# Kernel tuning notes

Hardware: AMD Instinct MI355X
Metric: run time of the kernel (lower is better)

Reference implementation:

```python
import jax, jax.numpy as jnp
import numpy as np

BLANK = 0          # tf.nn.ctc_loss default blank_index (StringLookup reserves 0 for OOV)
PAD = 127          # padding_value = char_to_num.vocabulary_size()
NEG = -1e30        # log-space 'zero' (avoid -inf to keep grads NaN-free)
B, T, C, L = 1024, 256, 128, 32


def setup_inputs() -> dict:
    key = jax.random.key(0)
    k1, k2 = jax.random.split(key)
    # labels in [1, PAD-1]; none equal PAD so label_length == L (full-length labels)
    y_true = jax.random.randint(k1, (B, L), 1, PAD).astype(jnp.int32)
    y_pred = jax.random.normal(k2, (B, T, C), dtype=jnp.float32)
    return {"y_true": y_true, "y_pred": y_pred}


def _ctc_loss(y_true, y_pred):
    """Faithful jax version of tf.nn.ctc_loss(labels, logits, label_len, T,
    logits_time_major=False, blank_index=0): standard log-space alpha DP."""
    Bn, Tn, Cn = y_pred.shape
    Ln = y_true.shape[1]
    S = 2 * Ln + 1  # extended label length (blanks interleaved)

    logp = jax.nn.log_softmax(y_pred, axis=-1)                    # [B,T,C]

    # extended label sequence: blank, l1, blank, l2, ..., blank   # [B,S]
    ext = jnp.full((Bn, S), BLANK, dtype=y_true.dtype)
    ext = ext.at[:, 1::2].set(y_true)

    # log-probs gathered at extended-label symbols                # [B,T,S]
    lp_ext = jnp.take_along_axis(
        logp, jnp.broadcast_to(ext[:, None, :], (Bn, Tn, S)), axis=2)

    # label_length = count of non-padding entries (mirrors count_nonzero)
    label_len = jnp.sum(y_true != PAD, axis=1)                    # [B]

    # skip transition s-2 -> s allowed iff ext[s] is a non-blank differing
    # from ext[s-2]
    skip_ok = jnp.concatenate(
        [jnp.zeros((Bn, 2), bool),
         (ext[:, 2:] != BLANK) & (ext[:, 2:] != ext[:, :-2])], axis=1)  # [B,S]

    neg1 = jnp.full((Bn, 1), NEG, logp.dtype)
    neg2 = jnp.full((Bn, 2), NEG, logp.dtype)

    alpha0 = jnp.full((Bn, S), NEG, logp.dtype)
    alpha0 = alpha0.at[:, 0].set(lp_ext[:, 0, 0]).at[:, 1].set(lp_ext[:, 0, 1])

    def step(alpha, lp_t):  # alpha,[B,S]  lp_t,[B,S]
        a1 = jnp.concatenate([neg1, alpha[:, :-1]], axis=1)
        a2 = jnp.concatenate([neg2, alpha[:, :-2]], axis=1)
        a2 = jnp.where(skip_ok, a2, NEG)
        new = lp_t + jnp.logaddexp(jnp.logaddexp(alpha, a1), a2)
        return new, None

    lp_seq = jnp.transpose(lp_ext, (1, 0, 2))                     # [T,B,S]
    alphaT, _ = jax.lax.scan(step, alpha0, lp_seq[1:])            # [B,S]

    # total log-likelihood ends at last blank (2*len) or last label (2*len-1)
    bi = jnp.arange(Bn)
    e1 = 2 * label_len
    e2 = 2 * label_len - 1
    loglik = jnp.logaddexp(alphaT[bi, e1], alphaT[bi, e2])        # [B]
    return -loglik


def reference(y_true, y_pred):
    # The original layer returns y_pred and registers the loss via add_loss;
    # the compute-dominant quantity is the per-example CTC loss, returned here.
    return _ctc_loss(y_true, y_pred)
```

## Files before the change

kernel.cpp:

```cpp
#include <hip/hip_runtime.h>
#include <cstdint>


#define CTC_BLANK 0
#define CTC_PAD   127
#define NEG       (-1e30f)
#define LOG2E     1.44269504088896340736f
#define LN2       0.69314718055994530942f

constexpr int Bn = 1024, Tn = 256, Cn = 128, Ln = 32;
constexpr int NSLOT = Ln + 1;
constexpr int GSLOT = 34;
constexpr int GT_B  = GSLOT * Tn;

constexpr size_t WS_GT   = 0;
constexpr size_t WS_SLOT = (size_t)Bn * GT_B * 2;
constexpr size_t WS_S    = WS_SLOT + (size_t)Bn * Ln * 4;
constexpr size_t WS_NEED = WS_S + (size_t)Bn * 4;

__device__ __forceinline__ float fexp2(float x) { return __builtin_amdgcn_exp2f(x); }
__device__ __forceinline__ float flog2(float x) { return __builtin_amdgcn_logf(x); }

template <int CTRL>
__device__ __forceinline__ float dpp_add(float s) {
    int v = __builtin_amdgcn_update_dpp(0, __float_as_int(s), CTRL, 0xF, 0xF, true);
    return s + __int_as_float(v);
}
__device__ __forceinline__ float dpp_wave_shr1(float src, float old) {
    return __int_as_float(__builtin_amdgcn_update_dpp(
        __float_as_int(old), __float_as_int(src), 0x138, 0xF, 0xF, false));
}
__device__ __forceinline__ void gl_lds16(const float* g, float* l) {
    __builtin_amdgcn_global_load_lds(
        (const __attribute__((address_space(1))) uint32_t*)g,
        (__attribute__((address_space(3))) uint32_t*)l, 16, 0, 0);
}

__global__ __launch_bounds__(512, 8) void ctc_softmax_kernel(
        const int*   __restrict__ y_true,
        const float* __restrict__ y_pred,
        _Float16*    __restrict__ Gt,
        int*         __restrict__ slotO_arr,
        float*       __restrict__ Sglob)
{
    __shared__ int labels[Ln];
    __shared__ __align__(16) int cmap[Cn];
    __shared__ int used[Cn];
    __shared__ int wcnt[8];
    __shared__ float partS[16];

    const int b    = blockIdx.x;
    const int tid  = threadIdx.x;
    const int lane = tid & 63;
    const int wave = tid >> 6;
    const int half = lane >> 5;
    const int l32  = lane & 31;

    const float4* gsrc = (const float4*)(y_pred + (size_t)b * Tn * Cn);
    float4 xr0 = gsrc[tid];
    float4 xr1 = gsrc[512  + tid];
    float4 xr2 = gsrc[1024 + tid];
    float4 xr3 = gsrc[1536 + tid];

    if (tid < Ln) labels[tid] = y_true[b * Ln + tid];
    if (tid < Cn) used[tid] = 0;
    __syncthreads();
    if (tid == 0) used[CTC_BLANK] = 1;
    if (tid < Ln) used[labels[tid]] = 1;
    __syncthreads();
    {
        bool f = (tid < Cn) && (used[tid] != 0);
        unsigned long long m = __ballot(f);
        if (lane == 0) wcnt[wave] = __popcll(m);
        __syncthreads();
        int base = 0;
        for (int w = 0; w < wave; ++w) base += wcnt[w];
        if (tid < Cn)
            cmap[tid] = f ? (base + __popcll(m & ((1ull << lane) - 1ull))) : -1;
        __syncthreads();
    }

    const int4 cm = ((const int4*)cmap)[l32];
    _Float16* gt = Gt + (size_t)b * GT_B;
    const int rbase = tid >> 5;
    float acc = 0.f;

    #pragma unroll
    for (int j = 0; j < 16; ++j) {
        float4 x;
        if      ((j & 3) == 0) x = xr0;
        else if ((j & 3) == 1) x = xr1;
        else if ((j & 3) == 2) x = xr2;
        else                   x = xr3;
        if (j + 4 < 16) {
            float4 nx = gsrc[(j + 4) * 512 + tid];
            if      ((j & 3) == 0) xr0 = nx;
            else if ((j & 3) == 1) xr1 = nx;
            else if ((j & 3) == 2) xr2 = nx;
            else                   xr3 = nx;
        }
        const float e0 = x.x * LOG2E, e1 = x.y * LOG2E,
                    e2 = x.z * LOG2E, e3 = x.w * LOG2E;
        const int tcol = j * 16 + rbase;
        if (cm.x >= 0) gt[cm.x * Tn + tcol] = (_Float16)e0;
        if (cm.y >= 0) gt[cm.y * Tn + tcol] = (_Float16)e1;
        if (cm.z >= 0) gt[cm.z * Tn + tcol] = (_Float16)e2;
        if (cm.w >= 0) gt[cm.w * Tn + tcol] = (_Float16)e3;
        float s = fexp2(e0) + fexp2(e1) + fexp2(e2) + fexp2(e3);
        s = dpp_add<0x111>(s);
        s = dpp_add<0x112>(s);
        s = dpp_add<0x114>(s);
        s = dpp_add<0x118>(s);
        s = dpp_add<0x142>(s);
        acc += flog2(s);
    }
    if (l32 == 31) partS[wave * 2 + half] = acc;
    if (tid < Ln) slotO_arr[b * Ln + tid] = cmap[labels[tid]];
    __syncthreads();
    if (tid == 0) {
        float S = 0.f;
        #pragma unroll
        for (int j = 0; j < 16; ++j) S += partS[j];
        Sglob[b] = S;
    }
}

typedef __attribute__((ext_vector_type(4))) _Float16 h4;

__global__ __launch_bounds__(256) void ctc_dp_kernel(
        const int*      __restrict__ y_true,
        const _Float16* __restrict__ Gt,
        const int*      __restrict__ slotO_arr,
        const float*    __restrict__ Sglob,
        float*          __restrict__ out)
{
    const int wave = threadIdx.x >> 6;
    const int i    = threadIdx.x & 63;
    const int b    = blockIdx.x * 4 + wave;
    if (b >= Bn) return;

    const bool validO = (i < Ln);
    const bool validE = (i <= Ln);
    const int  myLab   = validO ? y_true[b * Ln + i] : -1;
    const int  prevLab = (i >= 1 && i < Ln) ? y_true[b * Ln + i - 1] : -1;
    const int  slotO   = validO ? slotO_arr[b * Ln + i] : 0;
    const bool skipO   = (i >= 1 && i < Ln) &&
                         (myLab != CTC_BLANK) && (myLab != prevLab);
    const int  len = __popcll(__ballot(validO && (myLab != CTC_PAD)));

    const _Float16* gB = Gt + (size_t)b * GT_B;
    const _Float16* gO = gB + slotO * Tn;

    float aE = (i == 0) ? (float)gB[0] : NEG;
    float aO = (i == 0) ? (float)gO[0] : NEG;

    auto step = [&](float lpB, float lpO) {
        const float aOup = dpp_wave_shr1(aO, NEG);
        const float m  = fmaxf(aE, aOup);
        const float e1 = fexp2(aE - m);
        const float e2 = fexp2(aOup - m);
        const float sE = e1 + e2;
        const float nE = lpB + m + flog2(sE);
        const float m3 = fmaxf(aO, m);
        const float nO = lpO + m3 +
            flog2(fexp2(aO - m3) + (skipO ? sE : e1) * fexp2(m - m3));
        aE = validE ? nE : NEG;
        aO = validO ? nO : NEG;
    };

    h4 vB0 = *(const h4*)(gB),     vB1 = *(const h4*)(gB + 4);
    h4 vO0 = *(const h4*)(gO),     vO1 = *(const h4*)(gO + 4);
    {
        h4 nB0 = *(const h4*)(gB + 8),  nB1 = *(const h4*)(gB + 12);
        h4 nO0 = *(const h4*)(gO + 8),  nO1 = *(const h4*)(gO + 12);
        #pragma unroll
        for (int k = 1; k < 4; ++k) step((float)vB0[k], (float)vO0[k]);
        #pragma unroll
        for (int k = 0; k < 4; ++k) step((float)vB1[k], (float)vO1[k]);
        vB0 = nB0; vB1 = nB1; vO0 = nO0; vO1 = nO1;
    }
    for (int g = 1; g < 31; ++g) {
        h4 nB0 = *(const h4*)(gB + 8 * (g + 1));
        h4 nB1 = *(const h4*)(gB + 8 * (g + 1) + 4);
        h4 nO0 = *(const h4*)(gO + 8 * (g + 1));
        h4 nO1 = *(const h4*)(gO + 8 * (g + 1) + 4);
        #pragma unroll
        for (int k = 0; k < 4; ++k) step((float)vB0[k], (float)vO0[k]);
        #pragma unroll
        for (int k = 0; k < 4; ++k) step((float)vB1[k], (float)vO1[k]);
        vB0 = nB0; vB1 = nB1; vO0 = nO0; vO1 = nO1;
    }
    #pragma unroll
    for (int k = 0; k < 4; ++k) step((float)vB0[k], (float)vO0[k]);
    #pragma unroll
    for (int k = 0; k < 4; ++k) step((float)vB1[k], (float)vO1[k]);

    const float v1 = __shfl(aE, len, 64);
    const float v2 = __shfl(aO, len - 1, 64);
    if (i == 0) {
        const float S  = Sglob[b];
        const float mm = fmaxf(v1, v2);
        const float L2 = mm + flog2(fexp2(v1 - mm) + fexp2(v2 - mm));
        out[b] = LN2 * (S - L2);
    }
}

constexpr int CR  = 16;
constexpr int NCH = Tn / CR;
constexpr int CF  = CR * Cn;

__global__ __launch_bounds__(512, 8) void ctc_fused_fallback(
        const int*   __restrict__ y_true,
        const float* __restrict__ y_pred,
        float*       __restrict__ out)
{
    __shared__ __align__(16) float raw[2][CF];
    __shared__ _Float16 Gc[Tn * NSLOT];
    __shared__ int   labels[Ln];
    __shared__ __align__(16) int cmap[Cn];
    __shared__ int   used[Cn];
    __shared__ int   wcnt[8];
    __shared__ float partS[16];

    const int b    = blockIdx.x;
    const int tid  = threadIdx.x;
    const int lane = tid & 63;
    const int wave = tid >> 6;

    const float* gbase = y_pred + (size_t)b * Tn * Cn;
    auto stage = [&](int c, int buf) {
        gl_lds16(gbase + c * CF + tid * 4, &raw[buf][wave * 256]);
    };
    stage(0, 0);

    if (tid < Ln) labels[tid] = y_true[b * Ln + tid];
    if (tid < Cn) used[tid] = 0;
    __syncthreads();
    if (tid == 0) used[CTC_BLANK] = 1;
    if (tid < Ln) used[labels[tid]] = 1;
    __syncthreads();
    {
        bool f = (tid < Cn) && (used[tid] != 0);
        unsigned long long m = __ballot(f);
        if (lane == 0) wcnt[wave] = __popcll(m);
        __syncthreads();
        int base = 0;
        for (int w = 0; w < wave; ++w) base += wcnt[w];
        if (tid < Cn)
            cmap[tid] = f ? (base + __popcll(m & ((1ull << lane) - 1ull))) : -1;
        __syncthreads();
    }

    const int half = lane >> 5;
    const int l32  = lane & 31;
    const int4 cm  = ((const int4*)cmap)[l32];
    float acc = 0.f;

    const int  i      = lane;
    const bool validO = (i < Ln);
    const bool validE = (i <= Ln);
    const int  myLab   = validO ? labels[i] : -1;
    const int  prevLab = (i >= 1 && i < Ln) ? labels[i - 1] : -1;
    const int  slotO   = validO ? cmap[myLab] : 0;
    const bool skipO   = (i >= 1 && i < Ln) &&
                         (myLab != CTC_BLANK) && (myLab != prevLab);
    const int  len = __popcll(__ballot(validO && (myLab != CTC_PAD)));
    float aE = NEG, aO = NEG;

    auto dp_chunk = [&](int t0, int t1) {
        int t = t0;
        if (t == 0) {
            aE = (i == 0) ? (float)Gc[0]     : NEG;
            aO = (i == 0) ? (float)Gc[slotO] : NEG;
            t = 1;
        }
        float pB[2], pO[2];
        const int ta = t, tb = (t + 1 < t1) ? t + 1 : t1 - 1;
        pB[0] = (float)Gc[ta * NSLOT]; pO[0] = (float)Gc[ta * NSLOT + slotO];
        pB[1] = (float)Gc[tb * NSLOT]; pO[1] = (float)Gc[tb * NSLOT + slotO];
        int k = 0;
        #pragma unroll 2
        for (; t < t1; ++t) {
            const float lpB = pB[k], lpO = pO[k];
            const int tp = (t + 2 < t1) ? t + 2 : t1 - 1;
            pB[k] = (float)Gc[tp * NSLOT];
            pO[k] = (float)Gc[tp * NSLOT + slotO];
            k ^= 1;
            const float aOup = dpp_wave_shr1(aO, NEG);
            const float m  = fmaxf(aE, aOup);
            const float e1 = fexp2(aE - m);
            const float e2 = fexp2(aOup - m);
            const float sE = e1 + e2;
            const float nE = lpB + m + flog2(sE);
            const float m3 = fmaxf(aO, m);
            const float nO = lpO + m3 +
                flog2(fexp2(aO - m3) + (skipO ? sE : e1) * fexp2(m - m3));
            aE = validE ? nE : NEG;
            aO = validO ? nO : NEG;
        }
    };

    for (int c = 0; c < NCH; ++c) {
        if (c + 1 < NCH) stage(c + 1, (c + 1) & 1);
        if (wave == 0 && c > 0) dp_chunk((c - 1) * CR, c * CR);
        __builtin_amdgcn_sched_barrier(0);
        if (c + 1 < NCH) asm volatile("s_waitcnt vmcnt(1)" ::: "memory");
        else             asm volatile("s_waitcnt vmcnt(0)" ::: "memory");
        __builtin_amdgcn_sched_barrier(0);
        {
            const int rl = 2 * wave + half;
            const int r  = c * CR + rl;
            const float4 x = ((const float4*)&raw[c & 1][rl * Cn])[l32];
            const float e0 = x.x * LOG2E, e1 = x.y * LOG2E,
                        e2 = x.z * LOG2E, e3 = x.w * LOG2E;
            if (cm.x >= 0) Gc[r * NSLOT + cm.x] = (_Float16)e0;
            if (cm.y >= 0) Gc[r * NSLOT + cm.y] = (_Float16)e1;
            if (cm.z >= 0) Gc[r * NSLOT + cm.z] = (_Float16)e2;
            if (cm.w >= 0) Gc[r * NSLOT + cm.w] = (_Float16)e3;
            float s = fexp2(e0) + fexp2(e1) + fexp2(e2) + fexp2(e3);
            s = dpp_add<0x111>(s);
            s = dpp_add<0x112>(s);
            s = dpp_add<0x114>(s);
            s = dpp_add<0x118>(s);
            s = dpp_add<0x142>(s);
            acc += flog2(s);
        }
        if (c == NCH - 1 && l32 == 31) partS[wave * 2 + half] = acc;
        asm volatile("s_waitcnt lgkmcnt(0)" ::: "memory");
        __builtin_amdgcn_s_barrier();
    }

    if (wave == 0) {
        dp_chunk(Tn - CR, Tn);
        const float v1 = __shfl(aE, len, 64);
        const float v2 = __shfl(aO, len - 1, 64);
        if (i == 0) {
            float S = 0.f;
            #pragma unroll
            for (int j = 0; j < 16; ++j) S += partS[j];
            const float mm = fmaxf(v1, v2);
            const float L2 = mm + flog2(fexp2(v1 - mm) + fexp2(v2 - mm));
            out[b] = LN2 * (S - L2);
        }
    }
}

extern "C" void kernel_launch(void* const* d_in, const int* in_sizes, int n_in,
                              void* d_out, int out_size, void* d_ws, size_t ws_size,
                              hipStream_t stream) {
    const int*   y_true = (const int*)d_in[0];
    const float* y_pred = (const float*)d_in[1];
    float*       out    = (float*)d_out;
    if (d_ws != nullptr && ws_size >= WS_NEED) {
        _Float16* Gt    = (_Float16*)((char*)d_ws + WS_GT);
        int*      slotO = (int*)((char*)d_ws + WS_SLOT);
        float*    Sg    = (float*)((char*)d_ws + WS_S);
        ctc_softmax_kernel<<<Bn, 512, 0, stream>>>(y_true, y_pred, Gt, slotO, Sg);
        ctc_dp_kernel<<<Bn / 4, 256, 0, stream>>>(y_true, Gt, slotO, Sg, out);
    } else {
        ctc_fused_fallback<<<Bn, 512, 0, stream>>>(y_true, y_pred, out);
    }
}
```

Baseline: 227.3 us.

## Stage gathered log-probs in LDS and write time-chunked tiles to global

```diff
diff --git a/kernel.cpp b/kernel.cpp
--- a/kernel.cpp
+++ b/kernel.cpp
@@ -10,8 +10,8 @@
 
 constexpr int Bn = 1024, Tn = 256, Cn = 128, Ln = 32;
 constexpr int NSLOT = Ln + 1;
-constexpr int GSLOT = 34;
-constexpr int GT_B  = GSLOT * Tn;
+constexpr int GS    = 34;
+constexpr int GT_B  = 16 * GS * 16;
 
 constexpr size_t WS_GT   = 0;
 constexpr size_t WS_SLOT = (size_t)Bn * GT_B * 2;
@@ -43,6 +43,7 @@
         int*         __restrict__ slotO_arr,
         float*       __restrict__ Sglob)
 {
+    __shared__ _Float16 Gc[Tn * GS];
     __shared__ int labels[Ln];
     __shared__ __align__(16) int cmap[Cn];
     __shared__ int used[Cn];
@@ -81,7 +82,6 @@
     }
 
     const int4 cm = ((const int4*)cmap)[l32];
-    _Float16* gt = Gt + (size_t)b * GT_B;
     const int rbase = tid >> 5;
     float acc = 0.f;
 
@@ -102,10 +102,10 @@
         const float e0 = x.x * LOG2E, e1 = x.y * LOG2E,
                     e2 = x.z * LOG2E, e3 = x.w * LOG2E;
         const int tcol = j * 16 + rbase;
-        if (cm.x >= 0) gt[cm.x * Tn + tcol] = (_Float16)e0;
-        if (cm.y >= 0) gt[cm.y * Tn + tcol] = (_Float16)e1;
-        if (cm.z >= 0) gt[cm.z * Tn + tcol] = (_Float16)e2;
-        if (cm.w >= 0) gt[cm.w * Tn + tcol] = (_Float16)e3;
+        if (cm.x >= 0) Gc[tcol * GS + cm.x] = (_Float16)e0;
+        if (cm.y >= 0) Gc[tcol * GS + cm.y] = (_Float16)e1;
+        if (cm.z >= 0) Gc[tcol * GS + cm.z] = (_Float16)e2;
+        if (cm.w >= 0) Gc[tcol * GS + cm.w] = (_Float16)e3;
         float s = fexp2(e0) + fexp2(e1) + fexp2(e2) + fexp2(e3);
         s = dpp_add<0x111>(s);
         s = dpp_add<0x112>(s);
@@ -117,6 +117,23 @@
     if (l32 == 31) partS[wave * 2 + half] = acc;
     if (tid < Ln) slotO_arr[b * Ln + tid] = cmap[labels[tid]];
     __syncthreads();
+
+    {
+        const uint16_t* GcU = (const uint16_t*)Gc;
+        const int tc = tid >> 5;
+        for (int s = (tid & 31); s < NSLOT; s += 32) {
+            uint32_t w[8];
+            #pragma unroll
+            for (int k = 0; k < 8; ++k) {
+                const uint32_t lo = GcU[(tc * 16 + 2 * k)     * GS + s];
+                const uint32_t hi = GcU[(tc * 16 + 2 * k + 1) * GS + s];
+                w[k] = lo | (hi << 16);
+            }
+            uint4* dst = (uint4*)(Gt + (size_t)b * GT_B + tc * (GS * 16) + s * 16);
+            dst[0] = make_uint4(w[0], w[1], w[2], w[3]);
+            dst[1] = make_uint4(w[4], w[5], w[6], w[7]);
+        }
+    }
     if (tid == 0) {
         float S = 0.f;
         #pragma unroll
@@ -125,7 +142,7 @@
     }
 }
 
-typedef __attribute__((ext_vector_type(4))) _Float16 h4;
+typedef __attribute__((ext_vector_type(8))) _Float16 h8;
 
 __global__ __launch_bounds__(256) void ctc_dp_kernel(
         const int*      __restrict__ y_true,
@@ -149,10 +166,10 @@
     const int  len = __popcll(__ballot(validO && (myLab != CTC_PAD)));
 
     const _Float16* gB = Gt + (size_t)b * GT_B;
-    const _Float16* gO = gB + slotO * Tn;
-
-    float aE = (i == 0) ? (float)gB[0] : NEG;
-    float aO = (i == 0) ? (float)gO[0] : NEG;
+    const int oOff = slotO * 16;
+
+    float aE = (i == 0) ? (float)gB[0]    : NEG;
+    float aO = (i == 0) ? (float)gB[oOff] : NEG;
 
     auto step = [&](float lpB, float lpO) {
         const float aOup = dpp_wave_shr1(aO, NEG);
@@ -168,32 +185,28 @@
         aO = validO ? nO : NEG;
     };
 
-    h4 vB0 = *(const h4*)(gB),     vB1 = *(const h4*)(gB + 4);
-    h4 vO0 = *(const h4*)(gO),     vO1 = *(const h4*)(gO + 4);
+    auto ldB = [&](int g) -> h8 {
+        return *(const h8*)(gB + (g >> 1) * (GS * 16) + (g & 1) * 8);
+    };
+    auto ldO = [&](int g) -> h8 {
+        return *(const h8*)(gB + oOff + (g >> 1) * (GS * 16) + (g & 1) * 8);
+    };
+
+    h8 vB = ldB(0), vO = ldO(0);
     {
-        h4 nB0 = *(const h4*)(gB + 8),  nB1 = *(const h4*)(gB + 12);
-        h4 nO0 = *(const h4*)(gO + 8),  nO1 = *(const h4*)(gO + 12);
+        h8 nB = ldB(1), nO8 = ldO(1);
         #pragma unroll
-        for (int k = 1; k < 4; ++k) step((float)vB0[k], (float)vO0[k]);
+        for (int k = 1; k < 8; ++k) step((float)vB[k], (float)vO[k]);
+        vB = nB; vO = nO8;
+    }
+    for (int g = 1; g < 31; ++g) {
+        h8 nB = ldB(g + 1), nO8 = ldO(g + 1);
         #pragma unroll
-        for (int k = 0; k < 4; ++k) step((float)vB1[k], (float)vO1[k]);
-        vB0 = nB0; vB1 = nB1; vO0 = nO0; vO1 = nO1;
-    }
-    for (int g = 1; g < 31; ++g) {
-        h4 nB0 = *(const h4*)(gB + 8 * (g + 1));
-        h4 nB1 = *(const h4*)(gB + 8 * (g + 1) + 4);
-        h4 nO0 = *(const h4*)(gO + 8 * (g + 1));
-        h4 nO1 = *(const h4*)(gO + 8 * (g + 1) + 4);
-        #pragma unroll
-        for (int k = 0; k < 4; ++k) step((float)vB0[k], (float)vO0[k]);
-        #pragma unroll
-        for (int k = 0; k < 4; ++k) step((float)vB1[k], (float)vO1[k]);
-        vB0 = nB0; vB1 = nB1; vO0 = nO0; vO1 = nO1;
+        for (int k = 0; k < 8; ++k) step((float)vB[k], (float)vO[k]);
+        vB = nB; vO = nO8;
     }
     #pragma unroll
-    for (int k = 0; k < 4; ++k) step((float)vB0[k], (float)vO0[k]);
-    #pragma unroll
-    for (int k = 0; k < 4; ++k) step((float)vB1[k], (float)vO1[k]);
+    for (int k = 0; k < 8; ++k) step((float)vB[k], (float)vO[k]);
 
     const float v1 = __shfl(aE, len, 64);
     const float v2 = __shfl(aO, len - 1, 64);
```

Result: faster. 214.8 us (-5.5%).
